# Kernel optimization log

Hardware: AMD Instinct MI355X
Metric: run time of the kernel (lower is better)

## Reference

```python
import jax, jax.numpy as jnp
import numpy as np

HIDDEN = 2048
NUM_HEADS = 16
NUM_KV_HEADS = 16
QK_NOPE = 128
QK_ROPE = 64
HEAD_DIM = QK_NOPE + QK_ROPE  # 192
V_HEAD = 128
KV_LORA = 512
Q_LORA = 1536
EPS = 1e-6


def rmsnorm(x, w):
    var = jnp.mean(x * x, axis=-1, keepdims=True)
    return x * jax.lax.rsqrt(var + EPS) * w


def setup_inputs() -> dict:
    key = jax.random.key(0)
    ks = jax.random.split(key, 8)
    s = lambda fan_in: 1.0 / np.sqrt(fan_in)
    return {
        "hidden_states": jax.random.normal(ks[0], (2, 2048, HIDDEN), jnp.float32),
        # weights stored as [in, out] so forward is x @ W
        "q_a_w": jax.random.normal(ks[1], (HIDDEN, Q_LORA), jnp.float32) * s(HIDDEN),
        "q_a_ln_w": jnp.ones((Q_LORA,), jnp.float32),
        "q_b_w": jax.random.normal(ks[2], (Q_LORA, NUM_HEADS * HEAD_DIM), jnp.float32) * s(Q_LORA),
        "kv_a_w": jax.random.normal(ks[3], (HIDDEN, KV_LORA + NUM_KV_HEADS * QK_ROPE), jnp.float32) * s(HIDDEN),
        "kv_a_ln_w": jnp.ones((KV_LORA,), jnp.float32),
        "kv_b_w": jax.random.normal(ks[4], (KV_LORA, NUM_KV_HEADS * (QK_NOPE + V_HEAD)), jnp.float32) * s(KV_LORA),
        "o_w": jax.random.normal(ks[5], (NUM_HEADS * V_HEAD, HIDDEN), jnp.float32) * s(NUM_HEADS * V_HEAD),
    }


def reference(hidden_states, q_a_w, q_a_ln_w, q_b_w, kv_a_w, kv_a_ln_w, kv_b_w, o_w):
    B, T, _ = hidden_states.shape
    # Q path: low-rank down-proj -> RMSNorm -> up-proj
    q = rmsnorm(hidden_states @ q_a_w, q_a_ln_w) @ q_b_w
    q = q.reshape(B, T, NUM_HEADS, HEAD_DIM)  # [B,T,H,192]

    # KV path: joint down-proj producing latent + rope slice
    kv_raw = hidden_states @ kv_a_w
    kv_latent = rmsnorm(kv_raw[..., :KV_LORA], kv_a_ln_w)
    k_rope = kv_raw[..., KV_LORA:].reshape(B, T, NUM_KV_HEADS, QK_ROPE)
    kv = (kv_latent @ kv_b_w).reshape(B, T, NUM_KV_HEADS, QK_NOPE + V_HEAD)
    k_nope = kv[..., :QK_NOPE]
    v = kv[..., QK_NOPE:]  # [B,T,Hkv,128]

    # NOTE: the original forward computes RoPE cos/sin but never applies the
    # rotation; q_rope/k_rope are used as-is (faithfully reproduced here).
    k = jnp.concatenate([k_nope, k_rope], axis=-1)  # [B,T,Hkv,192]
    # num_kv_groups == 1, so no repeat_interleave needed

    scale = 1.0 / jnp.sqrt(jnp.float32(HEAD_DIM))
    scores = jnp.einsum("bqhd,bkhd->bhqk", q, k) * scale  # [B,H,T,T]
    causal = jnp.tril(jnp.ones((T, T), bool))
    scores = jnp.where(causal, scores, jnp.finfo(scores.dtype).min)
    probs = jax.nn.softmax(scores, axis=-1)
    attn = jnp.einsum("bhqk,bkhd->bqhd", probs, v)  # [B,T,H,128]
    attn = attn.reshape(B, T, NUM_HEADS * V_HEAD)
    return attn @ o_w
```

## Files before the change

kernel.cpp:

```cpp
#include <hip/hip_runtime.h>
#include <cstdint>
#include <cstddef>

typedef unsigned short u16;
typedef short short8 __attribute__((ext_vector_type(8)));
typedef float f32x4 __attribute__((ext_vector_type(4)));

#define B_   2
#define T_   2048
#define H_   16
#define HID_ 2048
#define DQK_ 192
#define DV_  128
#define AW_  3072

__device__ __forceinline__ float bf2f(u16 u) {
  unsigned int v = ((unsigned int)u) << 16;
  return __builtin_bit_cast(float, v);
}
__device__ __forceinline__ u16 f2bf(float f) {
  unsigned int u = __builtin_bit_cast(unsigned int, f);
  u += 0x7fff + ((u >> 16) & 1);
  return (u16)(u >> 16);
}
__device__ __forceinline__ void load_lds16(const void* g, void* l) {
  __builtin_amdgcn_global_load_lds((const __attribute__((address_space(1))) void*)g,
                                   (__attribute__((address_space(3))) void*)l, 16, 0, 0);
}

__global__ __launch_bounds__(256) void cast_f32_bf16(const float* __restrict__ x,
                                                     u16* __restrict__ y) {
  size_t i = ((size_t)blockIdx.x * 256 + threadIdx.x) * 8;
  float4 a = *(const float4*)&x[i];
  float4 b = *(const float4*)&x[i + 4];
  u16 r[8];
  r[0] = f2bf(a.x); r[1] = f2bf(a.y); r[2] = f2bf(a.z); r[3] = f2bf(a.w);
  r[4] = f2bf(b.x); r[5] = f2bf(b.y); r[6] = f2bf(b.z); r[7] = f2bf(b.w);
  *(uint4*)&y[i] = *(const uint4*)&r[0];
}

__global__ __launch_bounds__(256) void transpose_cast_k(const float* __restrict__ W,
                                                        u16* __restrict__ Wt,
                                                        int K, int N) {
  __shared__ u16 tile[32][33];
  int n0 = blockIdx.x * 32, k0 = blockIdx.y * 32;
  int tx = threadIdx.x & 31, ty = threadIdx.x >> 5;
#pragma unroll
  for (int i = 0; i < 32; i += 8)
    tile[ty + i][tx] = f2bf(W[(size_t)(k0 + ty + i) * N + n0 + tx]);
  __syncthreads();
#pragma unroll
  for (int i = 0; i < 32; i += 8)
    Wt[(size_t)(n0 + ty + i) * K + k0 + tx] = tile[tx][ty + i];
}

__global__ __launch_bounds__(256) void rmsnorm_dual(const u16* __restrict__ qa,
                                                    const float* __restrict__ w1,
                                                    u16* __restrict__ out1,
                                                    const float* __restrict__ w2,
                                                    u16* __restrict__ out2) {
  __shared__ float red[4];
  const int row = blockIdx.x, tid = threadIdx.x;
  {
    const u16* x = qa + (size_t)row * AW_;
    float ss = 0.f;
    for (int i = tid * 8; i < 1536; i += 2048) {
      uint4 v = *(const uint4*)&x[i];
      const u16* p = (const u16*)&v;
#pragma unroll
      for (int e = 0; e < 8; ++e) { float f = bf2f(p[e]); ss += f * f; }
    }
#pragma unroll
    for (int m = 32; m >= 1; m >>= 1) ss += __shfl_xor(ss, m);
    if ((tid & 63) == 0) red[tid >> 6] = ss;
    __syncthreads();
    ss = red[0] + red[1] + red[2] + red[3];
    float inv = rsqrtf(ss / 1536.f + 1e-6f);
    u16* o = out1 + (size_t)row * 1536;
    for (int i = tid * 8; i < 1536; i += 2048) {
      uint4 v = *(const uint4*)&x[i];
      const u16* p = (const u16*)&v;
      u16 r8[8];
#pragma unroll
      for (int e = 0; e < 8; ++e) r8[e] = f2bf(bf2f(p[e]) * inv * w1[i + e]);
      *(uint4*)&o[i] = *(const uint4*)&r8[0];
    }
  }
  __syncthreads();
  {
    const u16* x = qa + (size_t)row * AW_ + 1536;
    float ss = 0.f;
    for (int i = tid * 8; i < 512; i += 2048) {
      uint4 v = *(const uint4*)&x[i];
      const u16* p = (const u16*)&v;
#pragma unroll
      for (int e = 0; e < 8; ++e) { float f = bf2f(p[e]); ss += f * f; }
    }
#pragma unroll
    for (int m = 32; m >= 1; m >>= 1) ss += __shfl_xor(ss, m);
    if ((tid & 63) == 0) red[tid >> 6] = ss;
    __syncthreads();
    ss = red[0] + red[1] + red[2] + red[3];
    float inv = rsqrtf(ss / 512.f + 1e-6f);
    u16* o = out2 + (size_t)row * 512;
    for (int i = tid * 8; i < 512; i += 2048) {
      uint4 v = *(const uint4*)&x[i];
      const u16* p = (const u16*)&v;
      u16 r8[8];
#pragma unroll
      for (int e = 0; e < 8; ++e) r8[e] = f2bf(bf2f(p[e]) * inv * w2[i + e]);
      *(uint4*)&o[i] = *(const uint4*)&r8[0];
    }
  }
}

template <int EPI>
__global__ __launch_bounds__(512) void gemm256(const u16* __restrict__ A,
                                               const u16* __restrict__ Bt,
                                               void* __restrict__ Cout,
                                               u16* __restrict__ Vt2,
                                               int M, int N, int K) {
  __shared__ u16 As[2][256 * 64];
  __shared__ u16 Bs[2][256 * 64];
  const int nbx = N >> 8;
  const int bx = blockIdx.x % nbx, by = blockIdx.x / nbx;
  const int m0 = by << 8, n0 = bx << 8;
  const int tid = threadIdx.x, w = tid >> 6, lane = tid & 63;
  const int wm = w >> 2, wn = w & 3;
  const int llo = lane & 15, lhi = lane >> 4;
  f32x4 acc[8][4] = {};

  const u16* srcp[8];
  int dsto[8];
#pragma unroll
  for (int jl = 0; jl < 2; ++jl) {
    int c = jl * 512 + tid;
    int i = c >> 3, sl = c & 7;
    { int r = ((i >> 6) << 7) + (i & 63);
      srcp[jl] = A + (size_t)(m0 + r) * K + ((sl ^ (r & 7)) << 3);
      dsto[jl] = (r * 8 + sl) * 8; }
    { int r = ((i >> 5) << 6) + (i & 31);
      srcp[2 + jl] = Bt + (size_t)(n0 + r) * K + ((sl ^ (r & 7)) << 3);
      dsto[2 + jl] = (r * 8 + sl) * 8; }
    { int r = ((i >> 5) << 6) + 32 + (i & 31);
      srcp[4 + jl] = Bt + (size_t)(n0 + r) * K + ((sl ^ (r & 7)) << 3);
      dsto[4 + jl] = (r * 8 + sl) * 8; }
    { int r = ((i >> 6) << 7) + 64 + (i & 63);
      srcp[6 + jl] = A + (size_t)(m0 + r) * K + ((sl ^ (r & 7)) << 3);
      dsto[6 + jl] = (r * 8 + sl) * 8; }
  }
#define STG(j, kt, buf)                                                        \
  load_lds16(srcp[j] + (size_t)(kt) * 64,                                      \
             ((j) < 2 || (j) >= 6) ? &As[(buf)][dsto[j]] : &Bs[(buf)][dsto[j]])

  auto rdA = [&](int buf, int mi, int ks) {
    int r = wm * 128 + mi * 16 + llo;
    return *(const short8*)&As[buf][r * 64 + (((ks * 4 + lhi) ^ (r & 7)) << 3)];
  };
  auto rdB = [&](int buf, int nj, int ks) {
    int r = wn * 64 + nj * 16 + llo;
    return *(const short8*)&Bs[buf][r * 64 + (((ks * 4 + lhi) ^ (r & 7)) << 3)];
  };

  const int NT = K >> 6;
#pragma unroll
  for (int j = 0; j < 8; ++j) STG(j, 0, 0);

  short8 af[4][2], bf[2][2];
  for (int kt = 0; kt < NT; ++kt) {
    const int cur = kt & 1, nxt = cur ^ 1;
    const bool hn = (kt + 1 < NT);
    asm volatile("s_waitcnt vmcnt(4)" ::: "memory");
    __builtin_amdgcn_s_barrier();
#pragma unroll
    for (int mi = 0; mi < 4; ++mi) { af[mi][0] = rdA(cur, mi, 0); af[mi][1] = rdA(cur, mi, 1); }
#pragma unroll
    for (int nj = 0; nj < 2; ++nj) { bf[nj][0] = rdB(cur, nj, 0); bf[nj][1] = rdB(cur, nj, 1); }
    if (hn) { STG(0, kt + 1, nxt); STG(1, kt + 1, nxt); }
    __builtin_amdgcn_s_setprio(1);
#pragma unroll
    for (int mi = 0; mi < 4; ++mi)
#pragma unroll
      for (int nj = 0; nj < 2; ++nj)
#pragma unroll
        for (int ks = 0; ks < 2; ++ks)
          acc[mi][nj] = __builtin_amdgcn_mfma_f32_16x16x32_bf16(af[mi][ks], bf[nj][ks], acc[mi][nj], 0, 0, 0);
    __builtin_amdgcn_s_setprio(0);
    if (hn) asm volatile("s_waitcnt vmcnt(4)" ::: "memory");
    else    asm volatile("s_waitcnt vmcnt(2)" ::: "memory");
    __builtin_amdgcn_s_barrier();
#pragma unroll
    for (int nj = 0; nj < 2; ++nj) { bf[nj][0] = rdB(cur, 2 + nj, 0); bf[nj][1] = rdB(cur, 2 + nj, 1); }
    if (hn) { STG(2, kt + 1, nxt); STG(3, kt + 1, nxt); }
    __builtin_amdgcn_s_setprio(1);
#pragma unroll
    for (int mi = 0; mi < 4; ++mi)
#pragma unroll
      for (int nj = 0; nj < 2; ++nj)
#pragma unroll
        for (int ks = 0; ks < 2; ++ks)
          acc[mi][2 + nj] = __builtin_amdgcn_mfma_f32_16x16x32_bf16(af[mi][ks], bf[nj][ks], acc[mi][2 + nj], 0, 0, 0);
    __builtin_amdgcn_s_setprio(0);
    if (hn) asm volatile("s_waitcnt vmcnt(4)" ::: "memory");
    else    asm volatile("s_waitcnt vmcnt(0)" ::: "memory");
    __builtin_amdgcn_s_barrier();
#pragma unroll
    for (int mi = 0; mi < 4; ++mi) { af[mi][0] = rdA(cur, 4 + mi, 0); af[mi][1] = rdA(cur, 4 + mi, 1); }
    if (hn) { STG(4, kt + 1, nxt); STG(5, kt + 1, nxt); }
    __builtin_amdgcn_s_setprio(1);
#pragma unroll
    for (int mi = 0; mi < 4; ++mi)
#pragma unroll
      for (int nj = 0; nj < 2; ++nj)
#pragma unroll
        for (int ks = 0; ks < 2; ++ks)
          acc[4 + mi][2 + nj] = __builtin_amdgcn_mfma_f32_16x16x32_bf16(af[mi][ks], bf[nj][ks], acc[4 + mi][2 + nj], 0, 0, 0);
    __builtin_amdgcn_s_setprio(0);
#pragma unroll
    for (int nj = 0; nj < 2; ++nj) { bf[nj][0] = rdB(cur, nj, 0); bf[nj][1] = rdB(cur, nj, 1); }
    if (hn) { STG(6, kt + 1, nxt); STG(7, kt + 1, nxt); }
    __builtin_amdgcn_s_setprio(1);
#pragma unroll
    for (int mi = 0; mi < 4; ++mi)
#pragma unroll
      for (int nj = 0; nj < 2; ++nj)
#pragma unroll
        for (int ks = 0; ks < 2; ++ks)
          acc[4 + mi][nj] = __builtin_amdgcn_mfma_f32_16x16x32_bf16(af[mi][ks], bf[nj][ks], acc[4 + mi][nj], 0, 0, 0);
    __builtin_amdgcn_s_setprio(0);
  }
#undef STG

  const float scale = (EPI == 3) ? 0.10412163f : 1.0f;
  u16* C = (u16*)Cout;
#pragma unroll
  for (int mi = 0; mi < 8; ++mi)
#pragma unroll
    for (int nj = 0; nj < 4; ++nj) {
      u16 vals[4];
#pragma unroll
      for (int r = 0; r < 4; ++r) {
        vals[r] = f2bf(acc[mi][nj][r] * scale);
        C[(size_t)(m0 + wm * 128 + mi * 16 + lhi * 4 + r) * N + (n0 + wn * 64 + nj * 16 + llo)] =
            vals[r];
      }
      if constexpr (EPI == 2) {
        if (wn >= 2) {
          const int n = n0 + wn * 64 + nj * 16 + llo;
          const int mb = m0 + wm * 128 + mi * 16 + lhi * 4;
          const int bb = mb >> 11, t = mb & 2047;
          const int h = n >> 8, d = (n & 255) - 128;
          *(uint2*)&Vt2[((size_t)((bb << 4) + h) * 128 + d) * (size_t)T_ + t] =
              *(const uint2*)&vals[0];
        }
      }
    }
}

template <int EPI>
__global__ __launch_bounds__(256) void gemm_bt(const u16* __restrict__ A,
                                               const u16* __restrict__ Bt,
                                               void* __restrict__ Cout,
                                               int M, int N, int K) {
  __shared__ u16 As[3][128 * 32];
  __shared__ u16 Bs[3][128 * 32];
  const int nbx = N >> 7;
  const int bx = blockIdx.x % nbx, by = blockIdx.x / nbx;
  const int m0 = by << 7, n0 = bx << 7;
  const int tid = threadIdx.x, w = tid >> 6, lane = tid & 63;
  const int wr = w >> 1, wc = w & 1;
  const int llo = lane & 15, lhi = lane >> 4;
  f32x4 acc[4][4] = {};

  const int c0 = tid, c1 = tid + 256;
  const int ar0 = c0 >> 2, s0_ = c0 & 3;
  const int ar1 = c1 >> 2, s1_ = c1 & 3;
  const u16* Asrc0 = A + (size_t)(m0 + ar0) * K + (s0_ ^ ((ar0 >> 1) & 3)) * 8;
  const u16* Asrc1 = A + (size_t)(m0 + ar1) * K + (s1_ ^ ((ar1 >> 1) & 3)) * 8;
  const u16* Bsrc0 = Bt + (size_t)(n0 + ar0) * K + (s0_ ^ ((ar0 >> 1) & 3)) * 8;
  const u16* Bsrc1 = Bt + (size_t)(n0 + ar1) * K + (s1_ ^ ((ar1 >> 1) & 3)) * 8;

  int aoff[4], boff[4];
#pragma unroll
  for (int i = 0; i < 4; ++i) {
    int rowa = wr * 64 + i * 16 + llo;
    aoff[i] = (rowa * 4 + (lhi ^ ((rowa >> 1) & 3))) * 8;
    int rowb = wc * 64 + i * 16 + llo;
    boff[i] = (rowb * 4 + (lhi ^ ((rowb >> 1) & 3))) * 8;
  }

#define STAGE_KT(kt, buf)                                   \
  do {                                                      \
    int k0_ = (kt) << 5;                                    \
    load_lds16(Asrc0 + k0_, &As[(buf)][c0 * 8]);            \
    load_lds16(Asrc1 + k0_, &As[(buf)][c1 * 8]);            \
    load_lds16(Bsrc0 + k0_, &Bs[(buf)][c0 * 8]);            \
    load_lds16(Bsrc1 + k0_, &Bs[(buf)][c1 * 8]);            \
  } while (0)

  const int NT = K >> 5;
  STAGE_KT(0, 0);
  STAGE_KT(1, 1);
  asm volatile("s_waitcnt vmcnt(4)" ::: "memory");
  __builtin_amdgcn_s_barrier();

  int cur = 0, nxt = 2;
  for (int kt = 0; kt < NT; ++kt) {
    if (kt + 2 < NT) STAGE_KT(kt + 2, nxt);
    short8 af[4], bfr[4];
#pragma unroll
    for (int i = 0; i < 4; ++i) af[i] = *(const short8*)&As[cur][aoff[i]];
#pragma unroll
    for (int j = 0; j < 4; ++j) bfr[j] = *(const short8*)&Bs[cur][boff[j]];
    __builtin_amdgcn_s_setprio(1);
#pragma unroll
    for (int i = 0; i < 4; ++i)
#pragma unroll
      for (int j = 0; j < 4; ++j)
        acc[i][j] = __builtin_amdgcn_mfma_f32_16x16x32_bf16(af[i], bfr[j], acc[i][j], 0, 0, 0);
    __builtin_amdgcn_s_setprio(0);
    if (kt + 2 < NT) asm volatile("s_waitcnt vmcnt(4)" ::: "memory");
    else             asm volatile("s_waitcnt vmcnt(0)" ::: "memory");
    __builtin_amdgcn_s_barrier();
    cur = (cur == 2) ? 0 : cur + 1;
    nxt = (nxt == 2) ? 0 : nxt + 1;
  }
#undef STAGE_KT

  if constexpr (EPI == 0) {
    float* C = (float*)Cout;
#pragma unroll
    for (int i = 0; i < 4; ++i)
#pragma unroll
      for (int j = 0; j < 4; ++j)
#pragma unroll
        for (int r = 0; r < 4; ++r)
          C[(size_t)(m0 + wr * 64 + i * 16 + lhi * 4 + r) * N + (n0 + wc * 64 + j * 16 + llo)] =
              acc[i][j][r];
  } else {
    u16* C = (u16*)Cout;
#pragma unroll
    for (int i = 0; i < 4; ++i)
#pragma unroll
      for (int j = 0; j < 4; ++j)
#pragma unroll
        for (int r = 0; r < 4; ++r)
          C[(size_t)(m0 + wr * 64 + i * 16 + lhi * 4 + r) * N + (n0 + wc * 64 + j * 16 + llo)] =
              f2bf(acc[i][j][r]);
  }
}

__global__ __launch_bounds__(256, 2) void attn_k(const u16* __restrict__ q,
                                                 const u16* __restrict__ kv,
                                                 const u16* __restrict__ kvraw,
                                                 const u16* __restrict__ Vt,
                                                 u16* __restrict__ att) {
  constexpr int KLD = 192, VLD = 64, PLD = 64;
  __shared__ u16 Ks[2][64 * KLD];
  __shared__ u16 Vs[128 * VLD];
  __shared__ u16 Ps[64 * PLD];
  const int p = (int)blockIdx.x;
  const int xcd = p & 7, j = p >> 3;
  const int bh = xcd * 4 + (j & 3);
  const int pr = j >> 2;
  const int b = bh >> 4, h = bh & 15;
  const int bT = b * T_;
  const int tid = threadIdx.x, w = tid >> 6, lane = tid & 63;
  const int llo = lane & 15, lhi = lane >> 4;
  const u16* Vb = Vt + (size_t)bh * DV_ * T_;

  const u16* kbase[6]; int kstr[6];
#pragma unroll
  for (int ii = 0; ii < 6; ++ii) {
    int c = ii * 256 + tid;
    int rr = c / 24, chk = c - rr * 24;
    int sc = chk ^ (rr & 7);
    if (sc < 16) { kbase[ii] = kv + (size_t)(bT + rr) * 4096 + h * 256 + sc * 8; kstr[ii] = 4096; }
    else { kbase[ii] = kvraw + (size_t)(bT + rr) * AW_ + 2048 + h * 64 + (sc - 16) * 8; kstr[ii] = AW_; }
  }
  int voff[4];
#pragma unroll
  for (int ii = 0; ii < 4; ++ii) {
    int c = ii * 256 + tid;
    int rr = c >> 3, chk = c & 7;
    voff[ii] = rr * T_ + (chk ^ (rr & 7)) * 8;
  }

#pragma unroll
  for (int pass = 0; pass < 2; ++pass) {
    const int qt = pass == 0 ? 31 - pr : pr;
    const int q0 = qt * 64;
    const int rbase = q0 + w * 16;
    short8 qf[6];
#pragma unroll
    for (int kk = 0; kk < 6; ++kk)
      qf[kk] = *(const short8*)&q[(size_t)(bT + rbase + llo) * AW_ + h * DQK_ + kk * 32 + lhi * 8];
    f32x4 oacc[8] = {};
    float m_r[4], l_r[4];
#pragma unroll
    for (int r = 0; r < 4; ++r) { m_r[r] = -1e30f; l_r[r] = 0.f; }

#pragma unroll
    for (int ii = 0; ii < 6; ++ii)
      load_lds16(kbase[ii], &Ks[0][(ii * 256 + tid) * 8]);
    asm volatile("s_waitcnt vmcnt(0)" ::: "memory");
    __builtin_amdgcn_s_barrier();
    __builtin_amdgcn_sched_barrier(0);

    const u16* kp[6];
#pragma unroll
    for (int ii = 0; ii < 6; ++ii) kp[ii] = kbase[ii] + (size_t)64 * kstr[ii];
    const u16* vp[4];
#pragma unroll
    for (int ii = 0; ii < 4; ++ii) vp[ii] = Vb + voff[ii];

    const int nkt = qt + 1;
    int cur = 0;
    for (int kt = 0; kt < nkt; ++kt) {
      const int k0 = kt * 64;
      const bool hasNext = (kt + 1 < nkt);
#pragma unroll
      for (int ii = 0; ii < 4; ++ii)
        load_lds16(vp[ii], &Vs[(ii * 256 + tid) * 8]);
      if (hasNext) {
        u16* kd = Ks[cur ^ 1];
#pragma unroll
        for (int ii = 0; ii < 6; ++ii)
          load_lds16(kp[ii], &kd[(ii * 256 + tid) * 8]);
      }
#pragma unroll
      for (int ii = 0; ii < 4; ++ii) vp[ii] += 64;
#pragma unroll
      for (int ii = 0; ii < 6; ++ii) kp[ii] += (size_t)64 * kstr[ii];
      const u16* kbuf = Ks[cur];
      f32x4 s[4] = {};
      __builtin_amdgcn_s_setprio(1);
#pragma unroll
      for (int kk = 0; kk < 6; ++kk) {
        const int col = kk * 32 + lhi * 8;
        short8 kf[4];
#pragma unroll
        for (int j2 = 0; j2 < 4; ++j2) {
          const int row = j2 * 16 + llo;
          kf[j2] = *(const short8*)&kbuf[row * KLD + (col ^ ((row & 7) << 3))];
        }
#pragma unroll
        for (int j2 = 0; j2 < 4; ++j2)
          s[j2] = __builtin_amdgcn_mfma_f32_16x16x32_bf16(qf[kk], kf[j2], s[j2], 0, 0, 0);
      }
      __builtin_amdgcn_s_setprio(0);
      const bool needMask = (k0 + 63 > rbase);
#pragma unroll
      for (int r = 0; r < 4; ++r) {
        const int qrow = rbase + lhi * 4 + r;
        float sv[4];
#pragma unroll
        for (int j2 = 0; j2 < 4; ++j2) {
          float x = s[j2][r];
          if (needMask) { int kcol = k0 + j2 * 16 + llo; x = (kcol <= qrow) ? x : -1e30f; }
          sv[j2] = x;
        }
        float mx4 = fmaxf(fmaxf(sv[0], sv[1]), fmaxf(sv[2], sv[3]));
        if (!__all(mx4 - m_r[r] <= 8.f)) {
          float mx = mx4;
#pragma unroll
          for (int mk = 1; mk < 16; mk <<= 1) mx = fmaxf(mx, __shfl_xor(mx, mk));
          float mnew = fmaxf(m_r[r], mx);
          float alpha = exp2f(m_r[r] - mnew);
          m_r[r] = mnew;
          l_r[r] *= alpha;
#pragma unroll
          for (int jo = 0; jo < 8; ++jo) oacc[jo][r] *= alpha;
        }
        float rs = 0.f;
        const int prow = w * 16 + lhi * 4 + r;
#pragma unroll
        for (int j2 = 0; j2 < 4; ++j2) {
          float p2 = exp2f(sv[j2] - m_r[r]);
          rs += p2;
          int pcol = j2 * 16 + llo;
          Ps[prow * PLD + (pcol ^ ((prow & 7) << 3))] = f2bf(p2);
        }
        l_r[r] += rs;
      }
      if (hasNext) asm volatile("s_waitcnt vmcnt(6)" ::: "memory");
      else         asm volatile("s_waitcnt vmcnt(0)" ::: "memory");
      __builtin_amdgcn_s_barrier();
      __builtin_amdgcn_sched_barrier(0);
      __builtin_amdgcn_s_setprio(1);
#pragma unroll
      for (int kk2 = 0; kk2 < 2; ++kk2) {
        const int prow = w * 16 + llo;
        const int pcol = kk2 * 32 + lhi * 8;
        short8 pf = *(const short8*)&Ps[prow * PLD + (pcol ^ ((prow & 7) << 3))];
#pragma unroll
        for (int jo = 0; jo < 8; ++jo) {
          const int vrow = jo * 16 + llo;
          short8 vf = *(const short8*)&Vs[vrow * VLD + (pcol ^ ((vrow & 7) << 3))];
          oacc[jo] = __builtin_amdgcn_mfma_f32_16x16x32_bf16(pf, vf, oacc[jo], 0, 0, 0);
        }
      }
      __builtin_amdgcn_s_setprio(0);
      asm volatile("s_waitcnt vmcnt(0)" ::: "memory");
      __builtin_amdgcn_s_barrier();
      __builtin_amdgcn_sched_barrier(0);
      cur ^= 1;
    }
#pragma unroll
    for (int r = 0; r < 4; ++r) {
      float lr = l_r[r];
#pragma unroll
      for (int mk = 1; mk < 16; mk <<= 1) lr += __shfl_xor(lr, mk);
      const int qrow = rbase + lhi * 4 + r;
      const float linv = 1.f / lr;
#pragma unroll
      for (int jo = 0; jo < 8; ++jo)
        att[((size_t)bT + qrow) * (H_ * DV_) + h * DV_ + jo * 16 + llo] =
            f2bf(oacc[jo][r] * linv);
    }
  }
}

extern "C" void kernel_launch(void* const* d_in, const int* in_sizes, int n_in,
                              void* d_out, int out_size, void* d_ws, size_t ws_size,
                              hipStream_t stream) {
  const float* hs      = (const float*)d_in[0];
  const float* q_a_w   = (const float*)d_in[1];
  const float* q_a_ln  = (const float*)d_in[2];
  const float* q_b_w   = (const float*)d_in[3];
  const float* kv_a_w  = (const float*)d_in[4];
  const float* kv_a_ln = (const float*)d_in[5];
  const float* kv_b_w  = (const float*)d_in[6];
  const float* o_w     = (const float*)d_in[7];
  float* out = (float*)d_out;
  char* ws = (char*)d_ws;

  u16* hid  = (u16*)(ws + 0);
  u16* wt   = (u16*)(ws + 16777216);
  u16* qa   = (u16*)(ws + 29360128);
  u16* qan  = (u16*)(ws + 54525952);
  u16* qout = (u16*)(ws + 67108864);
  u16* att  = (u16*)(ws + 92274688);
  u16* kv   = (u16*)(ws + 109051904);
  u16* Vt   = (u16*)(ws + 142606336);
  u16* qan2 = (u16*)(ws + 159383552);

  cast_f32_bf16<<<4096, 256, 0, stream>>>(hs, hid);

  transpose_cast_k<<<dim3(1536 / 32, 2048 / 32), 256, 0, stream>>>(q_a_w, wt, 2048, 1536);
  transpose_cast_k<<<dim3(1536 / 32, 2048 / 32), 256, 0, stream>>>(kv_a_w, wt + (size_t)1536 * 2048, 2048, 1536);
  gemm256<1><<<(3072 / 256) * (4096 / 256), 512, 0, stream>>>(hid, wt, qa, nullptr, 4096, 3072, 2048);

  rmsnorm_dual<<<4096, 256, 0, stream>>>(qa, q_a_ln, qan, kv_a_ln, qan2);

  transpose_cast_k<<<dim3(3072 / 32, 1536 / 32), 256, 0, stream>>>(q_b_w, wt, 1536, 3072);
  gemm256<3><<<(3072 / 256) * (4096 / 256), 512, 0, stream>>>(qan, wt, qout, nullptr, 4096, 3072, 1536);

  transpose_cast_k<<<dim3(4096 / 32, 512 / 32), 256, 0, stream>>>(kv_b_w, wt, 512, 4096);
  gemm256<2><<<(4096 / 256) * (4096 / 256), 512, 0, stream>>>(qan2, wt, kv, Vt, 4096, 4096, 512);

  attn_k<<<512, 256, 0, stream>>>(qout, kv, qa, Vt, att);

  transpose_cast_k<<<dim3(2048 / 32, 2048 / 32), 256, 0, stream>>>(o_w, wt, 2048, 2048);
  gemm_bt<0><<<(2048 / 128) * (4096 / 128), 256, 0, stream>>>(att, wt, out, 4096, 2048, 2048);
}
```

Before: 315.5 us.

## Shrink attention KV tile to 32 and double-buffer V alongside K

The attention kernel now processes 32-key tiles instead of 64. V is double-buffered in LDS together with K, and both are prefetched one tile ahead. The mid-iteration wait and barrier between softmax and the PV matmul are removed, since each wave reads back only its own P rows. The P and V LDS swizzles are adapted to the 32-wide layout. This cuts LDS use and per-block latency, possibly allowing more resident blocks, in exchange for twice as many loop iterations and less MFMA work per synchronisation.

```diff
diff --git a/kernel.cpp b/kernel.cpp
--- a/kernel.cpp
+++ b/kernel.cpp
@@ -350,14 +350,14 @@
   }
 }
 
-__global__ __launch_bounds__(256, 2) void attn_k(const u16* __restrict__ q,
-                                                 const u16* __restrict__ kv,
-                                                 const u16* __restrict__ kvraw,
-                                                 const u16* __restrict__ Vt,
-                                                 u16* __restrict__ att) {
-  constexpr int KLD = 192, VLD = 64, PLD = 64;
-  __shared__ u16 Ks[2][64 * KLD];
-  __shared__ u16 Vs[128 * VLD];
+__global__ __launch_bounds__(256) void attn_k(const u16* __restrict__ q,
+                                              const u16* __restrict__ kv,
+                                              const u16* __restrict__ kvraw,
+                                              const u16* __restrict__ Vt,
+                                              u16* __restrict__ att) {
+  constexpr int KLD = 192, VLD = 32, PLD = 32;
+  __shared__ u16 Ks[2][32 * KLD];
+  __shared__ u16 Vs[2][128 * VLD];
   __shared__ u16 Ps[64 * PLD];
   const int p = (int)blockIdx.x;
   const int xcd = p & 7, j = p >> 3;
@@ -369,21 +369,21 @@
   const int llo = lane & 15, lhi = lane >> 4;
   const u16* Vb = Vt + (size_t)bh * DV_ * T_;
 
-  const u16* kbase[6]; int kstr[6];
-#pragma unroll
-  for (int ii = 0; ii < 6; ++ii) {
+  const u16* kbase[3]; int kstr[3];
+#pragma unroll
+  for (int ii = 0; ii < 3; ++ii) {
     int c = ii * 256 + tid;
     int rr = c / 24, chk = c - rr * 24;
     int sc = chk ^ (rr & 7);
     if (sc < 16) { kbase[ii] = kv + (size_t)(bT + rr) * 4096 + h * 256 + sc * 8; kstr[ii] = 4096; }
     else { kbase[ii] = kvraw + (size_t)(bT + rr) * AW_ + 2048 + h * 64 + (sc - 16) * 8; kstr[ii] = AW_; }
   }
-  int voff[4];
-#pragma unroll
-  for (int ii = 0; ii < 4; ++ii) {
+  const u16* vsrc[2];
+#pragma unroll
+  for (int ii = 0; ii < 2; ++ii) {
     int c = ii * 256 + tid;
-    int rr = c >> 3, chk = c & 7;
-    voff[ii] = rr * T_ + (chk ^ (rr & 7)) * 8;
+    int rr = c >> 2, sl = c & 3;
+    vsrc[ii] = Vb + (size_t)rr * T_ + (sl ^ ((rr >> 1) & 3)) * 8;
   }
 
 #pragma unroll
@@ -401,68 +401,60 @@
     for (int r = 0; r < 4; ++r) { m_r[r] = -1e30f; l_r[r] = 0.f; }
 
 #pragma unroll
-    for (int ii = 0; ii < 6; ++ii)
+    for (int ii = 0; ii < 3; ++ii)
       load_lds16(kbase[ii], &Ks[0][(ii * 256 + tid) * 8]);
+#pragma unroll
+    for (int ii = 0; ii < 2; ++ii)
+      load_lds16(vsrc[ii], &Vs[0][(ii * 256 + tid) * 8]);
     asm volatile("s_waitcnt vmcnt(0)" ::: "memory");
     __builtin_amdgcn_s_barrier();
     __builtin_amdgcn_sched_barrier(0);
 
-    const u16* kp[6];
-#pragma unroll
-    for (int ii = 0; ii < 6; ++ii) kp[ii] = kbase[ii] + (size_t)64 * kstr[ii];
-    const u16* vp[4];
-#pragma unroll
-    for (int ii = 0; ii < 4; ++ii) vp[ii] = Vb + voff[ii];
-
-    const int nkt = qt + 1;
+    const int nkt = 2 * qt + 2;
     int cur = 0;
     for (int kt = 0; kt < nkt; ++kt) {
-      const int k0 = kt * 64;
-      const bool hasNext = (kt + 1 < nkt);
-#pragma unroll
-      for (int ii = 0; ii < 4; ++ii)
-        load_lds16(vp[ii], &Vs[(ii * 256 + tid) * 8]);
-      if (hasNext) {
+      const int k0 = kt * 32;
+      if (kt + 1 < nkt) {
         u16* kd = Ks[cur ^ 1];
-#pragma unroll
-        for (int ii = 0; ii < 6; ++ii)
-          load_lds16(kp[ii], &kd[(ii * 256 + tid) * 8]);
+        u16* vd = Vs[cur ^ 1];
+#pragma unroll
+        for (int ii = 0; ii < 3; ++ii)
+          load_lds16(kbase[ii] + (size_t)(k0 + 32) * kstr[ii], &kd[(ii * 256 + tid) * 8]);
+#pragma unroll
+        for (int ii = 0; ii < 2; ++ii)
+          load_lds16(vsrc[ii] + k0 + 32, &vd[(ii * 256 + tid) * 8]);
       }
-#pragma unroll
-      for (int ii = 0; ii < 4; ++ii) vp[ii] += 64;
-#pragma unroll
-      for (int ii = 0; ii < 6; ++ii) kp[ii] += (size_t)64 * kstr[ii];
       const u16* kbuf = Ks[cur];
-      f32x4 s[4] = {};
+      f32x4 s[2] = {};
       __builtin_amdgcn_s_setprio(1);
 #pragma unroll
       for (int kk = 0; kk < 6; ++kk) {
         const int col = kk * 32 + lhi * 8;
-        short8 kf[4];
-#pragma unroll
-        for (int j2 = 0; j2 < 4; ++j2) {
+        short8 kf[2];
+#pragma unroll
+        for (int j2 = 0; j2 < 2; ++j2) {
           const int row = j2 * 16 + llo;
           kf[j2] = *(const short8*)&kbuf[row * KLD + (col ^ ((row & 7) << 3))];
         }
 #pragma unroll
-        for (int j2 = 0; j2 < 4; ++j2)
+        for (int j2 = 0; j2 < 2; ++j2)
           s[j2] = __builtin_amdgcn_mfma_f32_16x16x32_bf16(qf[kk], kf[j2], s[j2], 0, 0, 0);
       }
       __builtin_amdgcn_s_setprio(0);
-      const bool needMask = (k0 + 63 > rbase);
+      const bool needMask = (k0 + 31 > rbase);
 #pragma unroll
       for (int r = 0; r < 4; ++r) {
         const int qrow = rbase + lhi * 4 + r;
-        float sv[4];
-#pragma unroll
-        for (int j2 = 0; j2 < 4; ++j2) {
+        float sv[2];
+#pragma unroll
+        for (int j2 = 0; j2 < 2; ++j2) {
           float x = s[j2][r];
           if (needMask) { int kcol = k0 + j2 * 16 + llo; x = (kcol <= qrow) ? x : -1e30f; }
           sv[j2] = x;
         }
-        float mx4 = fmaxf(fmaxf(sv[0], sv[1]), fmaxf(sv[2], sv[3]));
-        if (!__all(mx4 - m_r[r] <= 8.f)) {
-          float mx = mx4;
+        float mx2 = fmaxf(sv[0], sv[1]);
+        if (!__all(mx2 - m_r[r] <= 8.f)) {
+          float mx = mx2;
 #pragma unroll
           for (int mk = 1; mk < 16; mk <<= 1) mx = fmaxf(mx, __shfl_xor(mx, mk));
           float mnew = fmaxf(m_r[r], mx);
@@ -472,31 +464,26 @@
 #pragma unroll
           for (int jo = 0; jo < 8; ++jo) oacc[jo][r] *= alpha;
         }
+        const int prow = w * 16 + lhi * 4 + r;
         float rs = 0.f;
-        const int prow = w * 16 + lhi * 4 + r;
-#pragma unroll
-        for (int j2 = 0; j2 < 4; ++j2) {
-          float p2 = exp2f(sv[j2] - m_r[r]);
-          rs += p2;
+#pragma unroll
+        for (int j2 = 0; j2 < 2; ++j2) {
+          float pv = exp2f(sv[j2] - m_r[r]);
+          rs += pv;
           int pcol = j2 * 16 + llo;
-          Ps[prow * PLD + (pcol ^ ((prow & 7) << 3))] = f2bf(p2);
+          int slot = pcol >> 3;
+          Ps[prow * PLD + ((slot ^ ((prow >> 1) & 3)) << 3) + (pcol & 7)] = f2bf(pv);
         }
         l_r[r] += rs;
       }
-      if (hasNext) asm volatile("s_waitcnt vmcnt(6)" ::: "memory");
-      else         asm volatile("s_waitcnt vmcnt(0)" ::: "memory");
-      __builtin_amdgcn_s_barrier();
-      __builtin_amdgcn_sched_barrier(0);
       __builtin_amdgcn_s_setprio(1);
-#pragma unroll
-      for (int kk2 = 0; kk2 < 2; ++kk2) {
+      {
         const int prow = w * 16 + llo;
-        const int pcol = kk2 * 32 + lhi * 8;
-        short8 pf = *(const short8*)&Ps[prow * PLD + (pcol ^ ((prow & 7) << 3))];
+        short8 pf = *(const short8*)&Ps[prow * PLD + ((lhi ^ ((prow >> 1) & 3)) << 3)];
 #pragma unroll
         for (int jo = 0; jo < 8; ++jo) {
           const int vrow = jo * 16 + llo;
-          short8 vf = *(const short8*)&Vs[vrow * VLD + (pcol ^ ((vrow & 7) << 3))];
+          short8 vf = *(const short8*)&Vs[cur][vrow * VLD + ((lhi ^ ((vrow >> 1) & 3)) << 3)];
           oacc[jo] = __builtin_amdgcn_mfma_f32_16x16x32_bf16(pf, vf, oacc[jo], 0, 0, 0);
         }
       }
```

After: 335.3 us. 1.06x slower.
